# Kernel tuning notes

Hardware: AMD Instinct MI355X
Metric: run time of the kernel (lower is better)

The kernel has to match this reference:

```python
import jax, jax.numpy as jnp
import numpy as np

INPUT_SIZE = 512
HIDDEN_SIZE = 512
BATCH = 128
SEQ_LEN = 512


def setup_inputs() -> dict:
    key = jax.random.key(0)
    k_xs, k_wih, k_whh, k_b, k_bn = jax.random.split(key, 5)
    lim = 1.0 / np.sqrt(HIDDEN_SIZE)  # equinox GRUCell init: U(-1/sqrt(H), 1/sqrt(H))
    xs = jax.random.normal(k_xs, (BATCH, SEQ_LEN, INPUT_SIZE), dtype=jnp.float32)
    weight_ih = jax.random.uniform(k_wih, (3 * HIDDEN_SIZE, INPUT_SIZE), minval=-lim, maxval=lim, dtype=jnp.float32)
    weight_hh = jax.random.uniform(k_whh, (3 * HIDDEN_SIZE, HIDDEN_SIZE), minval=-lim, maxval=lim, dtype=jnp.float32)
    bias = jax.random.uniform(k_b, (3 * HIDDEN_SIZE,), minval=-lim, maxval=lim, dtype=jnp.float32)
    bias_n = jax.random.uniform(k_bn, (HIDDEN_SIZE,), minval=-lim, maxval=lim, dtype=jnp.float32)
    return {"xs": xs, "weight_ih": weight_ih, "weight_hh": weight_hh, "bias": bias, "bias_n": bias_n}


def _gru_scan(xs, weight_ih, weight_hh, bias, bias_n):
    # xs: [B, T, I]. Precompute all input-side gates in one big GEMM: [B, T, 3H]
    igates_all = jnp.einsum('bti,gi->btg', xs, weight_ih) + bias
    B = xs.shape[0]
    H = weight_hh.shape[1]

    def step(h, ig_t):  # h: [B, H], ig_t: [B, 3H]
        hg = h @ weight_hh.T  # [B, 3H]
        ir, iz, in_ = jnp.split(ig_t, 3, axis=-1)
        hr, hz, hn = jnp.split(hg, 3, axis=-1)
        r = jax.nn.sigmoid(ir + hr)
        z = jax.nn.sigmoid(iz + hz)
        n = jnp.tanh(in_ + r * (hn + bias_n))
        h_new = n + z * (h - n)  # equinox GRUCell: new + inp*(hidden - new)
        return h_new, None

    init = jnp.zeros((B, H), dtype=xs.dtype)
    final_state, _ = jax.lax.scan(step, init, jnp.swapaxes(igates_all, 0, 1))  # scan over T
    return final_state  # [B, H]


def reference(xs, weight_ih, weight_hh, bias, bias_n):
    return _gru_scan(xs, weight_ih, weight_hh, bias, bias_n)
```

## Files before the change

### kernel.cpp

```cpp
#include <hip/hip_runtime.h>
#include <hip/hip_bf16.h>
#include <stdint.h>


static constexpr int INPUT = 512;
static constexpr int HID   = 512;
static constexpr int NB    = 128;
static constexpr int TLEN  = 512;
static constexpr int BGRPS = 8;
static constexpr int UGRPS = 32;

typedef __attribute__((ext_vector_type(4))) float f32x4;
typedef __attribute__((ext_vector_type(8))) short s16x8;

static __device__ __forceinline__ unsigned short f2bf(float f) {
  unsigned u = __builtin_bit_cast(unsigned, f);
  u += 0x7FFFu + ((u >> 16) & 1u);
  return (unsigned short)(u >> 16);
}

static __device__ __forceinline__ s16x8 cvt8(const float* p) {
  f32x4 a = *(const f32x4*)p;
  f32x4 b = *(const f32x4*)(p + 4);
  s16x8 r;
  r[0] = (short)f2bf(a[0]); r[1] = (short)f2bf(a[1]);
  r[2] = (short)f2bf(a[2]); r[3] = (short)f2bf(a[3]);
  r[4] = (short)f2bf(b[0]); r[5] = (short)f2bf(b[1]);
  r[6] = (short)f2bf(b[2]); r[7] = (short)f2bf(b[3]);
  return r;
}

__global__ __launch_bounds__(192, 2) void gru_fused(
    const float* __restrict__ xs, const float* __restrict__ wih,
    const float* __restrict__ whh, const float* __restrict__ bias,
    const float* __restrict__ bias_n, float* __restrict__ out,
    unsigned short* __restrict__ hbuf, unsigned int* __restrict__ flags)
{
  const int wg   = blockIdx.x;
  const int bgrp = wg & 7;
  const int ugrp = wg >> 3;
  const int b0   = bgrp * 16;
  const int u0   = ugrp * 16;
  const int tid  = threadIdx.x;
  const int g    = tid >> 6;
  const int lane = tid & 63;
  const int ln   = lane & 15;
  const int kg   = lane >> 4;

  const int rowW = g * HID + u0 + ln;
  s16x8 wa[16], wb[16];
#pragma unroll
  for (int ks = 0; ks < 16; ++ks) {
    const int k = ks * 32 + kg * 8;
    wa[ks] = cvt8(wih + (size_t)rowW * INPUT + k);
    wb[ks] = cvt8(whh + (size_t)rowW * HID + k);
  }
  const float bv = bias[rowW];
  const float bn = bias_n[u0 + ln];

  const float* xrow = xs + (size_t)(b0 + ln) * TLEN * INPUT + kg * 8;
  const int hoff = (b0 + ln) * HID + kg * 8;

  __shared__ float xch[2][4][16][16];

  float hold[4] = {0.f, 0.f, 0.f, 0.f};

  f32x4 acc_a = {bv, bv, bv, bv};
#pragma unroll
  for (int ks = 0; ks < 16; ++ks) {
    s16x8 xa = cvt8(xrow + ks * 32);
    acc_a = __builtin_amdgcn_mfma_f32_16x16x32_bf16(xa, wa[ks], acc_a, 0, 0, 0);
  }

  for (int t = 0; t < TLEN; ++t) {
    if (t > 0) {
      const unsigned* fp = &flags[bgrp * UGRPS + (lane & 31)];
      unsigned fv;
      do {
        fv = __hip_atomic_load(fp, __ATOMIC_RELAXED, __HIP_MEMORY_SCOPE_AGENT);
      } while (~__ballot(fv >= (unsigned)t));
      __builtin_amdgcn_sched_barrier(0);
    }

    const unsigned long long* hb =
        (const unsigned long long*)(hbuf + (size_t)(t & 1) * (NB * HID) + hoff);
    unsigned long long q0[16], q1[16];
#pragma unroll
    for (int ks = 0; ks < 16; ++ks) {
      q0[ks] = __hip_atomic_load(hb + ks * 8,     __ATOMIC_RELAXED, __HIP_MEMORY_SCOPE_AGENT);
      q1[ks] = __hip_atomic_load(hb + ks * 8 + 1, __ATOMIC_RELAXED, __HIP_MEMORY_SCOPE_AGENT);
    }

    f32x4 acc_b0 = {0.f, 0.f, 0.f, 0.f}, acc_b1 = {0.f, 0.f, 0.f, 0.f};
#pragma unroll
    for (int ks = 0; ks < 16; ks += 2) {
      union { unsigned long long q[2]; s16x8 s; } ua, ub;
      ua.q[0] = q0[ks];     ua.q[1] = q1[ks];
      ub.q[0] = q0[ks + 1]; ub.q[1] = q1[ks + 1];
      acc_b0 = __builtin_amdgcn_mfma_f32_16x16x32_bf16(ua.s, wb[ks],     acc_b0, 0, 0, 0);
      acc_b1 = __builtin_amdgcn_mfma_f32_16x16x32_bf16(ub.s, wb[ks + 1], acc_b1, 0, 0, 0);
    }
    f32x4 acc_b = acc_b0 + acc_b1;

    float (*xc)[16][16] = xch[t & 1];
    if (g == 0)      { f32x4 s = acc_a + acc_b; *(f32x4*)&xc[0][ln][kg * 4] = s; }
    else if (g == 1) { f32x4 s = acc_a + acc_b; *(f32x4*)&xc[1][ln][kg * 4] = s; }
    else             { *(f32x4*)&xc[2][ln][kg * 4] = acc_a;
                       *(f32x4*)&xc[3][ln][kg * 4] = acc_b; }
    __syncthreads();
    f32x4 Sr  = *(const f32x4*)&xc[0][ln][kg * 4];
    f32x4 Sz  = *(const f32x4*)&xc[1][ln][kg * 4];
    f32x4 Snx = *(const f32x4*)&xc[2][ln][kg * 4];
    f32x4 Snh = *(const f32x4*)&xc[3][ln][kg * 4];

    float hnew[4];
#pragma unroll
    for (int i = 0; i < 4; ++i) {
      float r = 1.f / (1.f + __expf(-Sr[i]));
      float z = 1.f / (1.f + __expf(-Sz[i]));
      float pre = Snx[i] + r * (Snh[i] + bn);
      float e = __expf(2.f * pre);
      float n = 1.f - 2.f / (e + 1.f);
      hnew[i] = n + z * (hold[i] - n);
      hold[i] = hnew[i];
    }

    if (t == TLEN - 1) {
      if (g == 0) {
#pragma unroll
        for (int i = 0; i < 4; ++i)
          out[(size_t)(b0 + kg * 4 + i) * HID + u0 + ln] = hnew[i];
      }
    } else {
      if (g == 0) {
        unsigned short* hbn = hbuf + (size_t)((t + 1) & 1) * (NB * HID);
#pragma unroll
        for (int i = 0; i < 4; ++i) {
          int v  = (int)f2bf(hnew[i]);
          int o1 = __shfl_xor(v, 1);
          unsigned int p = (unsigned int)(v & 0xffff) | ((unsigned int)(o1 & 0xffff) << 16);
          unsigned int o2 = (unsigned int)__shfl_xor((int)p, 2);
          if ((ln & 3) == 0) {
            unsigned long long q = (unsigned long long)p | ((unsigned long long)o2 << 32);
            __hip_atomic_store(
                (unsigned long long*)(hbn + (size_t)(b0 + kg * 4 + i) * HID + u0 + ln),
                q, __ATOMIC_RELAXED, __HIP_MEMORY_SCOPE_AGENT);
          }
        }
        asm volatile("s_waitcnt vmcnt(0)" ::: "memory");
        if (tid == 0)
          __hip_atomic_store(&flags[bgrp * UGRPS + ugrp], (unsigned)(t + 1),
                             __ATOMIC_RELAXED, __HIP_MEMORY_SCOPE_AGENT);
      }

      acc_a = (f32x4){bv, bv, bv, bv};
      const float* xp = xrow + (size_t)(t + 1) * INPUT;
#pragma unroll
      for (int ks = 0; ks < 16; ++ks) {
        s16x8 xa = cvt8(xp + ks * 32);
        acc_a = __builtin_amdgcn_mfma_f32_16x16x32_bf16(xa, wa[ks], acc_a, 0, 0, 0);
      }
    }
  }
}

extern "C" void kernel_launch(void* const* d_in, const int* in_sizes, int n_in,
                              void* d_out, int out_size, void* d_ws, size_t ws_size,
                              hipStream_t stream) {
  const float* xs     = (const float*)d_in[0];
  const float* wih    = (const float*)d_in[1];
  const float* whh    = (const float*)d_in[2];
  const float* bias   = (const float*)d_in[3];
  const float* bias_n = (const float*)d_in[4];
  float* out = (float*)d_out;

  const size_t hbuf_bytes = (size_t)2 * NB * HID * sizeof(unsigned short);
  const size_t flg_bytes  = (size_t)BGRPS * UGRPS * sizeof(unsigned int);
  unsigned short* hbuf  = (unsigned short*)d_ws;
  unsigned int*   flags = (unsigned int*)((char*)d_ws + hbuf_bytes);

  hipMemsetAsync(d_ws, 0, hbuf_bytes + flg_bytes, stream);

  gru_fused<<<dim3(BGRPS * UGRPS), dim3(192), 0, stream>>>(
      xs, wih, whh, bias, bias_n, out, hbuf, flags);
}
```

Measured before the change: 3.553 ms.

## Replace per-step flag polling with step-tagged hidden-state words

Adds a kernel in which each hidden value is stored as a 32-bit word: the bf16 value in the low half and the step number in the high half. Consumers spin on the data itself until every word carries the expected tag, so the separate flag write, the vmcnt wait and the second load round are gone. The cost is double the bytes per hidden-state read and larger spin loads on every poll iteration. The bf16 conversion is also switched to the packed v_cvt_pk_bf16_f32 instruction, and the old flag-based kernel is kept as a fallback for small workspaces.

```diff
diff --git a/kernel.cpp b/kernel.cpp
--- a/kernel.cpp
+++ b/kernel.cpp
@@ -22,15 +22,151 @@
 static __device__ __forceinline__ s16x8 cvt8(const float* p) {
   f32x4 a = *(const f32x4*)p;
   f32x4 b = *(const f32x4*)(p + 4);
-  s16x8 r;
-  r[0] = (short)f2bf(a[0]); r[1] = (short)f2bf(a[1]);
-  r[2] = (short)f2bf(a[2]); r[3] = (short)f2bf(a[3]);
-  r[4] = (short)f2bf(b[0]); r[5] = (short)f2bf(b[1]);
-  r[6] = (short)f2bf(b[2]); r[7] = (short)f2bf(b[3]);
-  return r;
-}
-
-__global__ __launch_bounds__(192, 2) void gru_fused(
+  unsigned r0, r1, r2, r3;
+  asm("v_cvt_pk_bf16_f32 %0, %1, %2" : "=v"(r0) : "v"(a[0]), "v"(a[1]));
+  asm("v_cvt_pk_bf16_f32 %0, %1, %2" : "=v"(r1) : "v"(a[2]), "v"(a[3]));
+  asm("v_cvt_pk_bf16_f32 %0, %1, %2" : "=v"(r2) : "v"(b[0]), "v"(b[1]));
+  asm("v_cvt_pk_bf16_f32 %0, %1, %2" : "=v"(r3) : "v"(b[2]), "v"(b[3]));
+  union { unsigned u[4]; s16x8 s; } r;
+  r.u[0] = r0; r.u[1] = r1; r.u[2] = r2; r.u[3] = r3;
+  return r.s;
+}
+
+
+__global__ __launch_bounds__(192, 1) void gru_tagged(
+    const float* __restrict__ xs, const float* __restrict__ wih,
+    const float* __restrict__ whh, const float* __restrict__ bias,
+    const float* __restrict__ bias_n, float* __restrict__ out,
+    unsigned int* __restrict__ th)
+{
+  const int wg   = blockIdx.x;
+  const int bgrp = wg & 7;
+  const int ugrp = wg >> 3;
+  const int b0   = bgrp * 16;
+  const int u0   = ugrp * 16;
+  const int tid  = threadIdx.x;
+  const int g    = tid >> 6;
+  const int lane = tid & 63;
+  const int ln   = lane & 15;
+  const int kg   = lane >> 4;
+
+  __shared__ float xch[2][4][16][16];
+
+  const int rowW = g * HID + u0 + ln;
+  s16x8 wa[16], wb[16];
+#pragma unroll
+  for (int ks = 0; ks < 16; ++ks) {
+    const int k = ks * 32 + kg * 8;
+    wa[ks] = cvt8(wih + (size_t)rowW * INPUT + k);
+    wb[ks] = cvt8(whh + (size_t)rowW * HID + k);
+  }
+  const float bv = bias[rowW];
+  const float bn = bias_n[u0 + ln];
+
+  const float* xrow = xrow = xs + (size_t)(b0 + ln) * TLEN * INPUT + kg * 8;
+
+  float hold[4] = {0.f, 0.f, 0.f, 0.f};
+
+  f32x4 acc_a = {bv, bv, bv, bv};
+#pragma unroll
+  for (int ks = 0; ks < 16; ++ks) {
+    s16x8 xa = cvt8(xrow + ks * 32);
+    acc_a = __builtin_amdgcn_mfma_f32_16x16x32_bf16(xa, wa[ks], acc_a, 0, 0, 0);
+  }
+
+  for (int t = 0; t < TLEN; ++t) {
+    const unsigned* hb = th + (size_t)(t & 1) * (NB * HID) + (b0 + ln) * HID + kg * 8;
+    const unsigned expv = (unsigned)t << 16;
+    unsigned w[16][8];
+    while (true) {
+#pragma unroll
+      for (int c = 0; c < 16; ++c)
+#pragma unroll
+        for (int j = 0; j < 8; ++j)
+          w[c][j] = __hip_atomic_load(hb + c * 32 + j,
+                                      __ATOMIC_RELAXED, __HIP_MEMORY_SCOPE_AGENT);
+      unsigned a0 = 0, a1 = 0, a2 = 0, a3 = 0;
+#pragma unroll
+      for (int c = 0; c < 16; c += 4)
+#pragma unroll
+        for (int j = 0; j < 8; ++j) {
+          a0 |= (w[c    ][j] ^ expv) & 0xffff0000u;
+          a1 |= (w[c + 1][j] ^ expv) & 0xffff0000u;
+          a2 |= (w[c + 2][j] ^ expv) & 0xffff0000u;
+          a3 |= (w[c + 3][j] ^ expv) & 0xffff0000u;
+        }
+      if (__ballot(((a0 | a1) | (a2 | a3)) != 0) == 0) break;
+    }
+    __builtin_amdgcn_sched_barrier(0);
+
+    f32x4 acc_b0 = {0.f, 0.f, 0.f, 0.f}, acc_b1 = {0.f, 0.f, 0.f, 0.f};
+#pragma unroll
+    for (int c = 0; c < 16; c += 2) {
+      union { unsigned u[4]; s16x8 s; } fa, fb;
+#pragma unroll
+      for (int q = 0; q < 4; ++q) {
+        fa.u[q] = __builtin_amdgcn_perm(w[c    ][2 * q + 1], w[c    ][2 * q], 0x05040100u);
+        fb.u[q] = __builtin_amdgcn_perm(w[c + 1][2 * q + 1], w[c + 1][2 * q], 0x05040100u);
+      }
+      acc_b0 = __builtin_amdgcn_mfma_f32_16x16x32_bf16(fa.s, wb[c],     acc_b0, 0, 0, 0);
+      acc_b1 = __builtin_amdgcn_mfma_f32_16x16x32_bf16(fb.s, wb[c + 1], acc_b1, 0, 0, 0);
+    }
+    f32x4 acc_b = acc_b0 + acc_b1;
+
+    float (*xc)[16][16] = xch[t & 1];
+    if (g == 0)      { f32x4 s = acc_a + acc_b; *(f32x4*)&xc[0][ln][kg * 4] = s; }
+    else if (g == 1) { f32x4 s = acc_a + acc_b; *(f32x4*)&xc[1][ln][kg * 4] = s; }
+    else             { *(f32x4*)&xc[2][ln][kg * 4] = acc_a;
+                       *(f32x4*)&xc[3][ln][kg * 4] = acc_b; }
+    __syncthreads();
+    f32x4 Sr  = *(const f32x4*)&xc[0][ln][kg * 4];
+    f32x4 Sz  = *(const f32x4*)&xc[1][ln][kg * 4];
+    f32x4 Snx = *(const f32x4*)&xc[2][ln][kg * 4];
+    f32x4 Snh = *(const f32x4*)&xc[3][ln][kg * 4];
+
+    float hnew[4];
+#pragma unroll
+    for (int i = 0; i < 4; ++i) {
+      float r = 1.f / (1.f + __expf(-Sr[i]));
+      float z = 1.f / (1.f + __expf(-Sz[i]));
+      float pre = Snx[i] + r * (Snh[i] + bn);
+      float e = __expf(2.f * pre);
+      float n = 1.f - 2.f / (e + 1.f);
+      hnew[i] = n + z * (hold[i] - n);
+      hold[i] = hnew[i];
+    }
+
+    if (t == TLEN - 1) {
+      if (g == 0) {
+#pragma unroll
+        for (int i = 0; i < 4; ++i)
+          out[(size_t)(b0 + kg * 4 + i) * HID + u0 + ln] = hnew[i];
+      }
+    } else {
+      if (g == 0) {
+        unsigned* thn = th + (size_t)((t + 1) & 1) * (NB * HID);
+        const unsigned tg = (unsigned)(t + 1) << 16;
+#pragma unroll
+        for (int i = 0; i < 4; ++i) {
+          unsigned wv = tg | (unsigned)f2bf(hnew[i]);
+          __hip_atomic_store(thn + (size_t)(b0 + kg * 4 + i) * HID + (u0 + ln), wv,
+                             __ATOMIC_RELAXED, __HIP_MEMORY_SCOPE_AGENT);
+        }
+      }
+
+      acc_a = (f32x4){bv, bv, bv, bv};
+      const float* xp = xrow + (size_t)(t + 1) * INPUT;
+#pragma unroll
+      for (int ks = 0; ks < 16; ++ks) {
+        s16x8 xa = cvt8(xp + ks * 32);
+        acc_a = __builtin_amdgcn_mfma_f32_16x16x32_bf16(xa, wa[ks], acc_a, 0, 0, 0);
+      }
+    }
+  }
+}
+
+
+__global__ __launch_bounds__(192, 2) void gru_flag(
     const float* __restrict__ xs, const float* __restrict__ wih,
     const float* __restrict__ whh, const float* __restrict__ bias,
     const float* __restrict__ bias_n, float* __restrict__ out,
@@ -62,7 +198,6 @@
   const int hoff = (b0 + ln) * HID + kg * 8;
 
   __shared__ float xch[2][4][16][16];
-
   float hold[4] = {0.f, 0.f, 0.f, 0.f};
 
   f32x4 acc_a = {bv, bv, bv, bv};
@@ -90,7 +225,6 @@
       q0[ks] = __hip_atomic_load(hb + ks * 8,     __ATOMIC_RELAXED, __HIP_MEMORY_SCOPE_AGENT);
       q1[ks] = __hip_atomic_load(hb + ks * 8 + 1, __ATOMIC_RELAXED, __HIP_MEMORY_SCOPE_AGENT);
     }
-
     f32x4 acc_b0 = {0.f, 0.f, 0.f, 0.f}, acc_b1 = {0.f, 0.f, 0.f, 0.f};
 #pragma unroll
     for (int ks = 0; ks < 16; ks += 2) {
@@ -174,13 +308,19 @@
   const float* bias_n = (const float*)d_in[4];
   float* out = (float*)d_out;
 
-  const size_t hbuf_bytes = (size_t)2 * NB * HID * sizeof(unsigned short);
-  const size_t flg_bytes  = (size_t)BGRPS * UGRPS * sizeof(unsigned int);
-  unsigned short* hbuf  = (unsigned short*)d_ws;
-  unsigned int*   flags = (unsigned int*)((char*)d_ws + hbuf_bytes);
-
-  hipMemsetAsync(d_ws, 0, hbuf_bytes + flg_bytes, stream);
-
-  gru_fused<<<dim3(BGRPS * UGRPS), dim3(192), 0, stream>>>(
-      xs, wih, whh, bias, bias_n, out, hbuf, flags);
-}
+  const size_t tag_bytes = (size_t)2 * NB * HID * sizeof(unsigned int);
+
+  if (ws_size >= tag_bytes) {
+    hipMemsetAsync(d_ws, 0, tag_bytes, stream);
+    gru_tagged<<<dim3(BGRPS * UGRPS), dim3(192), 0, stream>>>(
+        xs, wih, whh, bias, bias_n, out, (unsigned int*)d_ws);
+  } else {
+    const size_t hbuf_bytes = (size_t)2 * NB * HID * sizeof(unsigned short);
+    const size_t flg_bytes  = (size_t)BGRPS * UGRPS * sizeof(unsigned int);
+    unsigned short* hbuf  = (unsigned short*)d_ws;
+    unsigned int*   flags = (unsigned int*)((char*)d_ws + hbuf_bytes);
+    hipMemsetAsync(d_ws, 0, hbuf_bytes + flg_bytes, stream);
+    gru_flag<<<dim3(BGRPS * UGRPS), dim3(192), 0, stream>>>(
+        xs, wih, whh, bias, bias_n, out, hbuf, flags);
+  }
+}
```

New measurement: 9.120 ms. 2.57x slower.

## Interleave two independent batch groups per workgroup to hide recurrence latency

Applied to the files above, without the earlier changes.

Each workgroup now processes two batch groups (A and B) that share the same weight registers, alternating a GRU step for each. This halves the grid from 256 to 128 workgroups. While one batch group waits on its flag spin and cross-workgroup h exchange, the other group's step can proceed, so synchronisation latency is overlapped with useful work. The cost is twice the per-step serial work per workgroup and more register and LDS pressure, which may lengthen the critical path if the waits were not the bottleneck.

```diff
diff --git a/kernel.cpp b/kernel.cpp
--- a/kernel.cpp
+++ b/kernel.cpp
@@ -30,16 +30,117 @@
   return r;
 }
 
+static __device__ __forceinline__ void gru_step(
+    int t, int bgrp, int ugrp, int b0, int u0,
+    int g, int lane, int ln, int kg, int tid,
+    const s16x8* wa, const s16x8* wb, float bv, float bn,
+    const float* xrow, int hoff,
+    unsigned short* __restrict__ hbuf, unsigned int* __restrict__ flags,
+    float* __restrict__ out, float (*xch)[4][16][16],
+    float* hold, f32x4& acc_a)
+{
+  if (t > 0) {
+    const unsigned* fp = &flags[bgrp * UGRPS + (lane & 31)];
+    unsigned fv;
+    do {
+      fv = __hip_atomic_load(fp, __ATOMIC_RELAXED, __HIP_MEMORY_SCOPE_AGENT);
+    } while (~__ballot(fv >= (unsigned)t));
+    __builtin_amdgcn_sched_barrier(0);
+  }
+
+  const unsigned long long* hb =
+      (const unsigned long long*)(hbuf + (size_t)(t & 1) * (NB * HID) + hoff);
+  unsigned long long q0[16], q1[16];
+#pragma unroll
+  for (int ks = 0; ks < 16; ++ks) {
+    q0[ks] = __hip_atomic_load(hb + ks * 8,     __ATOMIC_RELAXED, __HIP_MEMORY_SCOPE_AGENT);
+    q1[ks] = __hip_atomic_load(hb + ks * 8 + 1, __ATOMIC_RELAXED, __HIP_MEMORY_SCOPE_AGENT);
+  }
+
+  f32x4 acc_b0 = {0.f, 0.f, 0.f, 0.f}, acc_b1 = {0.f, 0.f, 0.f, 0.f};
+#pragma unroll
+  for (int ks = 0; ks < 16; ks += 2) {
+    union { unsigned long long q[2]; s16x8 s; } ua, ub;
+    ua.q[0] = q0[ks];     ua.q[1] = q1[ks];
+    ub.q[0] = q0[ks + 1]; ub.q[1] = q1[ks + 1];
+    acc_b0 = __builtin_amdgcn_mfma_f32_16x16x32_bf16(ua.s, wb[ks],     acc_b0, 0, 0, 0);
+    acc_b1 = __builtin_amdgcn_mfma_f32_16x16x32_bf16(ub.s, wb[ks + 1], acc_b1, 0, 0, 0);
+  }
+  f32x4 acc_b = acc_b0 + acc_b1;
+
+  float (*xc)[16][16] = xch[t & 1];
+  if (g == 0)      { f32x4 s = acc_a + acc_b; *(f32x4*)&xc[0][ln][kg * 4] = s; }
+  else if (g == 1) { f32x4 s = acc_a + acc_b; *(f32x4*)&xc[1][ln][kg * 4] = s; }
+  else             { *(f32x4*)&xc[2][ln][kg * 4] = acc_a;
+                     *(f32x4*)&xc[3][ln][kg * 4] = acc_b; }
+  __syncthreads();
+  f32x4 Sr  = *(const f32x4*)&xc[0][ln][kg * 4];
+  f32x4 Sz  = *(const f32x4*)&xc[1][ln][kg * 4];
+  f32x4 Snx = *(const f32x4*)&xc[2][ln][kg * 4];
+  f32x4 Snh = *(const f32x4*)&xc[3][ln][kg * 4];
+
+  float hnew[4];
+#pragma unroll
+  for (int i = 0; i < 4; ++i) {
+    float r = 1.f / (1.f + __expf(-Sr[i]));
+    float z = 1.f / (1.f + __expf(-Sz[i]));
+    float pre = Snx[i] + r * (Snh[i] + bn);
+    float e = __expf(2.f * pre);
+    float n = 1.f - 2.f / (e + 1.f);
+    hnew[i] = n + z * (hold[i] - n);
+    hold[i] = hnew[i];
+  }
+
+  if (t == TLEN - 1) {
+    if (g == 0) {
+#pragma unroll
+      for (int i = 0; i < 4; ++i)
+        out[(size_t)(b0 + kg * 4 + i) * HID + u0 + ln] = hnew[i];
+    }
+  } else {
+    if (g == 0) {
+      unsigned short* hbn = hbuf + (size_t)((t + 1) & 1) * (NB * HID);
+#pragma unroll
+      for (int i = 0; i < 4; ++i) {
+        int v  = (int)f2bf(hnew[i]);
+        int o1 = __shfl_xor(v, 1);
+        unsigned int p = (unsigned int)(v & 0xffff) | ((unsigned int)(o1 & 0xffff) << 16);
+        unsigned int o2 = (unsigned int)__shfl_xor((int)p, 2);
+        if ((ln & 3) == 0) {
+          unsigned long long q = (unsigned long long)p | ((unsigned long long)o2 << 32);
+          __hip_atomic_store(
+              (unsigned long long*)(hbn + (size_t)(b0 + kg * 4 + i) * HID + u0 + ln),
+              q, __ATOMIC_RELAXED, __HIP_MEMORY_SCOPE_AGENT);
+        }
+      }
+      asm volatile("s_waitcnt vmcnt(0)" ::: "memory");
+      if (tid == 0)
+        __hip_atomic_store(&flags[bgrp * UGRPS + ugrp], (unsigned)(t + 1),
+                           __ATOMIC_RELAXED, __HIP_MEMORY_SCOPE_AGENT);
+    }
+
+    acc_a = (f32x4){bv, bv, bv, bv};
+    const float* xp = xrow + (size_t)(t + 1) * INPUT;
+#pragma unroll
+    for (int ks = 0; ks < 16; ++ks) {
+      s16x8 xa = cvt8(xp + ks * 32);
+      acc_a = __builtin_amdgcn_mfma_f32_16x16x32_bf16(xa, wa[ks], acc_a, 0, 0, 0);
+    }
+  }
+}
+
 __global__ __launch_bounds__(192, 2) void gru_fused(
     const float* __restrict__ xs, const float* __restrict__ wih,
     const float* __restrict__ whh, const float* __restrict__ bias,
     const float* __restrict__ bias_n, float* __restrict__ out,
     unsigned short* __restrict__ hbuf, unsigned int* __restrict__ flags)
 {
-  const int wg   = blockIdx.x;
-  const int bgrp = wg & 7;
-  const int ugrp = wg >> 3;
-  const int b0   = bgrp * 16;
+  const int w    = blockIdx.x;
+  const int bgA  = w & 3;
+  const int bgB  = 4 + (w & 3);
+  const int ugrp = w >> 2;
+  const int b0A  = bgA * 16;
+  const int b0B  = bgB * 16;
   const int u0   = ugrp * 16;
   const int tid  = threadIdx.x;
   const int g    = tid >> 6;
@@ -47,6 +148,9 @@
   const int ln   = lane & 15;
   const int kg   = lane >> 4;
 
+  __shared__ float xchA[2][4][16][16];
+  __shared__ float xchB[2][4][16][16];
+
   const int rowW = g * HID + u0 + ln;
   s16x8 wa[16], wb[16];
 #pragma unroll
@@ -58,109 +162,31 @@
   const float bv = bias[rowW];
   const float bn = bias_n[u0 + ln];
 
-  const float* xrow = xs + (size_t)(b0 + ln) * TLEN * INPUT + kg * 8;
-  const int hoff = (b0 + ln) * HID + kg * 8;
-
-  __shared__ float xch[2][4][16][16];
-
-  float hold[4] = {0.f, 0.f, 0.f, 0.f};
-
-  f32x4 acc_a = {bv, bv, bv, bv};
-#pragma unroll
-  for (int ks = 0; ks < 16; ++ks) {
-    s16x8 xa = cvt8(xrow + ks * 32);
-    acc_a = __builtin_amdgcn_mfma_f32_16x16x32_bf16(xa, wa[ks], acc_a, 0, 0, 0);
+  const float* xrowA = xs + (size_t)(b0A + ln) * TLEN * INPUT + kg * 8;
+  const float* xrowB = xs + (size_t)(b0B + ln) * TLEN * INPUT + kg * 8;
+  const int hoffA = (b0A + ln) * HID + kg * 8;
+  const int hoffB = (b0B + ln) * HID + kg * 8;
+
+  float holdA[4] = {0.f, 0.f, 0.f, 0.f};
+  float holdB[4] = {0.f, 0.f, 0.f, 0.f};
+
+  f32x4 accA = {bv, bv, bv, bv}, accB = {bv, bv, bv, bv};
+#pragma unroll
+  for (int ks = 0; ks < 16; ++ks) {
+    s16x8 xa = cvt8(xrowA + ks * 32);
+    accA = __builtin_amdgcn_mfma_f32_16x16x32_bf16(xa, wa[ks], accA, 0, 0, 0);
+  }
+#pragma unroll
+  for (int ks = 0; ks < 16; ++ks) {
+    s16x8 xb = cvt8(xrowB + ks * 32);
+    accB = __builtin_amdgcn_mfma_f32_16x16x32_bf16(xb, wa[ks], accB, 0, 0, 0);
   }
 
   for (int t = 0; t < TLEN; ++t) {
-    if (t > 0) {
-      const unsigned* fp = &flags[bgrp * UGRPS + (lane & 31)];
-      unsigned fv;
-      do {
-        fv = __hip_atomic_load(fp, __ATOMIC_RELAXED, __HIP_MEMORY_SCOPE_AGENT);
-      } while (~__ballot(fv >= (unsigned)t));
-      __builtin_amdgcn_sched_barrier(0);
-    }
-
-    const unsigned long long* hb =
-        (const unsigned long long*)(hbuf + (size_t)(t & 1) * (NB * HID) + hoff);
-    unsigned long long q0[16], q1[16];
-#pragma unroll
-    for (int ks = 0; ks < 16; ++ks) {
-      q0[ks] = __hip_atomic_load(hb + ks * 8,     __ATOMIC_RELAXED, __HIP_MEMORY_SCOPE_AGENT);
-      q1[ks] = __hip_atomic_load(hb + ks * 8 + 1, __ATOMIC_RELAXED, __HIP_MEMORY_SCOPE_AGENT);
-    }
-
-    f32x4 acc_b0 = {0.f, 0.f, 0.f, 0.f}, acc_b1 = {0.f, 0.f, 0.f, 0.f};
-#pragma unroll
-    for (int ks = 0; ks < 16; ks += 2) {
-      union { unsigned long long q[2]; s16x8 s; } ua, ub;
-      ua.q[0] = q0[ks];     ua.q[1] = q1[ks];
-      ub.q[0] = q0[ks + 1]; ub.q[1] = q1[ks + 1];
-      acc_b0 = __builtin_amdgcn_mfma_f32_16x16x32_bf16(ua.s, wb[ks],     acc_b0, 0, 0, 0);
-      acc_b1 = __builtin_amdgcn_mfma_f32_16x16x32_bf16(ub.s, wb[ks + 1], acc_b1, 0, 0, 0);
-    }
-    f32x4 acc_b = acc_b0 + acc_b1;
-
-    float (*xc)[16][16] = xch[t & 1];
-    if (g == 0)      { f32x4 s = acc_a + acc_b; *(f32x4*)&xc[0][ln][kg * 4] = s; }
-    else if (g == 1) { f32x4 s = acc_a + acc_b; *(f32x4*)&xc[1][ln][kg * 4] = s; }
-    else             { *(f32x4*)&xc[2][ln][kg * 4] = acc_a;
-                       *(f32x4*)&xc[3][ln][kg * 4] = acc_b; }
-    __syncthreads();
-    f32x4 Sr  = *(const f32x4*)&xc[0][ln][kg * 4];
-    f32x4 Sz  = *(const f32x4*)&xc[1][ln][kg * 4];
-    f32x4 Snx = *(const f32x4*)&xc[2][ln][kg * 4];
-    f32x4 Snh = *(const f32x4*)&xc[3][ln][kg * 4];
-
-    float hnew[4];
-#pragma unroll
-    for (int i = 0; i < 4; ++i) {
-      float r = 1.f / (1.f + __expf(-Sr[i]));
-      float z = 1.f / (1.f + __expf(-Sz[i]));
-      float pre = Snx[i] + r * (Snh[i] + bn);
-      float e = __expf(2.f * pre);
-      float n = 1.f - 2.f / (e + 1.f);
-      hnew[i] = n + z * (hold[i] - n);
-      hold[i] = hnew[i];
-    }
-
-    if (t == TLEN - 1) {
-      if (g == 0) {
-#pragma unroll
-        for (int i = 0; i < 4; ++i)
-          out[(size_t)(b0 + kg * 4 + i) * HID + u0 + ln] = hnew[i];
-      }
-    } else {
-      if (g == 0) {
-        unsigned short* hbn = hbuf + (size_t)((t + 1) & 1) * (NB * HID);
-#pragma unroll
-        for (int i = 0; i < 4; ++i) {
-          int v  = (int)f2bf(hnew[i]);
-          int o1 = __shfl_xor(v, 1);
-          unsigned int p = (unsigned int)(v & 0xffff) | ((unsigned int)(o1 & 0xffff) << 16);
-          unsigned int o2 = (unsigned int)__shfl_xor((int)p, 2);
-          if ((ln & 3) == 0) {
-            unsigned long long q = (unsigned long long)p | ((unsigned long long)o2 << 32);
-            __hip_atomic_store(
-                (unsigned long long*)(hbn + (size_t)(b0 + kg * 4 + i) * HID + u0 + ln),
-                q, __ATOMIC_RELAXED, __HIP_MEMORY_SCOPE_AGENT);
-          }
-        }
-        asm volatile("s_waitcnt vmcnt(0)" ::: "memory");
-        if (tid == 0)
-          __hip_atomic_store(&flags[bgrp * UGRPS + ugrp], (unsigned)(t + 1),
-                             __ATOMIC_RELAXED, __HIP_MEMORY_SCOPE_AGENT);
-      }
-
-      acc_a = (f32x4){bv, bv, bv, bv};
-      const float* xp = xrow + (size_t)(t + 1) * INPUT;
-#pragma unroll
-      for (int ks = 0; ks < 16; ++ks) {
-        s16x8 xa = cvt8(xp + ks * 32);
-        acc_a = __builtin_amdgcn_mfma_f32_16x16x32_bf16(xa, wa[ks], acc_a, 0, 0, 0);
-      }
-    }
+    gru_step(t, bgA, ugrp, b0A, u0, g, lane, ln, kg, tid,
+             wa, wb, bv, bn, xrowA, hoffA, hbuf, flags, out, xchA, holdA, accA);
+    gru_step(t, bgB, ugrp, b0B, u0, g, lane, ln, kg, tid,
+             wa, wb, bv, bn, xrowB, hoffB, hbuf, flags, out, xchB, holdB, accB);
   }
 }
 
@@ -181,6 +207,6 @@
 
   hipMemsetAsync(d_ws, 0, hbuf_bytes + flg_bytes, stream);
 
-  gru_fused<<<dim3(BGRPS * UGRPS), dim3(192), 0, stream>>>(
+  gru_fused<<<dim3(128), dim3(192), 0, stream>>>(
       xs, wih, whh, bias, bias_n, out, hbuf, flags);
 }
```

Result: slower. 10.71 ms (+201.5%).
